# Performance work log

Hardware: AMD Instinct MI355X
Metric: run time of the kernel (lower is better)

The kernel has to match this reference:

```python
import jax, jax.numpy as jnp
import numpy as np

B, S, D, H = 64, 2048, 512, 512


def setup_inputs() -> dict:
    key = jax.random.key(0)
    ks = jax.random.split(key, 8)
    inp = jax.random.normal(ks[0], (B, D), dtype=jnp.float32)
    context = jax.random.normal(ks[1], (B, S, D), dtype=jnp.float32)
    mask = jax.random.randint(ks[2], (B, S), 0, 2).astype(jnp.int32)
    alpha_mask = jax.random.uniform(ks[3], (B, S), dtype=jnp.float32)
    sd = 1.0 / np.sqrt(D)
    W_in = jax.random.uniform(ks[4], (H, D), minval=-sd, maxval=sd, dtype=jnp.float32)
    b_in = jnp.zeros((H,), dtype=jnp.float32)
    W_ctx = jax.random.uniform(ks[5], (H, D), minval=-sd, maxval=sd, dtype=jnp.float32)  # Conv1d k=1 == pointwise linear
    b_ctx = jnp.zeros((H,), dtype=jnp.float32)
    V = jax.random.uniform(ks[6], (H,), minval=-1.0, maxval=1.0, dtype=jnp.float32)
    return {"input": inp, "context": context, "alpha_mask": alpha_mask,
            "W_in": W_in, "b_in": b_in, "W_ctx": W_ctx, "b_ctx": b_ctx, "V": V,
            "mask": mask}


def reference(input, context, alpha_mask, W_in, b_in, W_ctx, b_ctx, V, mask):
    seq_len = context.shape[1]
    # input_linear: [B, H]
    inp = input @ W_in.T + b_in
    # context_linear (Conv1d kernel=1 over permuted context): [B, H, S]
    ctx = jnp.einsum('hd,bsd->bhs', W_ctx, context) + b_ctx[None, :, None]
    # additive attention energies: V . tanh(inp + ctx) -> [B, S]
    att = jnp.einsum('h,bhs->bs', V, jnp.tanh(inp[:, :, None] + ctx))
    # mask branching (faithful to the torch data-dependent branch, jit-safe):
    # if any(mask) and count(mask) == S: att[mask] = -inf; else: att = att * alpha_mask
    mb = mask != 0
    n_true = jnp.sum(mb)
    take_inf_branch = (n_true > 0) & (n_true == seq_len)
    att = jnp.where(take_inf_branch,
                    jnp.where(mb, -jnp.inf, att),
                    att * alpha_mask)
    alpha = jax.nn.softmax(att, axis=-1)  # [B, S]
    # context vector: bmm(ctx [B,H,S], alpha [B,S,1]) -> [B, H]
    hidden_state = jnp.einsum('bhs,bs->bh', ctx, alpha)
    return hidden_state, alpha
```

## Files before the change

### kernel.cpp

```cpp
#include <hip/hip_runtime.h>
#include <math.h>

#define B 64
#define S 2048
#define D 512
#define H 512

#define WSC 128

typedef _Float16 f16x8 __attribute__((ext_vector_type(8)));
typedef __fp16 fp16x2 __attribute__((ext_vector_type(2)));
typedef float f32x4 __attribute__((ext_vector_type(4)));

#define WS_PART_OFF (512 * 1024)
#define WS_CNT_OFF  (512 * 1024 + 2 * 1024 * 1024)

__global__ __launch_bounds__(256) void k_pack_wc(
        const float* __restrict__ Wc, _Float16* __restrict__ wsB,
        int* __restrict__ cnt) {
    if (blockIdx.x == 0 && threadIdx.x == 0) *cnt = 0;
    const int slot = blockIdx.x * 256 + threadIdx.x;
    const int st   = slot >> 11;
    const int rem  = slot & 2047;
    const int hg   = rem >> 6;
    const int lane = rem & 63;
    const int h  = hg * 16 + (lane & 15);
    const int k0 = st * 32 + (lane >> 4) * 8;
    const float* src = Wc + (size_t)h * D + k0;
    float4 f0 = *(const float4*)src;
    float4 f1 = *(const float4*)(src + 4);
    f16x8 v;
    v[0] = (_Float16)f0.x; v[1] = (_Float16)f0.y;
    v[2] = (_Float16)f0.z; v[3] = (_Float16)f0.w;
    v[4] = (_Float16)f1.x; v[5] = (_Float16)f1.y;
    v[6] = (_Float16)f1.z; v[7] = (_Float16)f1.w;
    *(f16x8*)(wsB + (size_t)slot * 8) = v;
}

__global__ __launch_bounds__(256) void k_mask_count(
        const int* __restrict__ mask, int* __restrict__ cnt) {
    const int base = blockIdx.x * 256 + threadIdx.x;
    int local = 0;
    for (int i = base; i < B * S; i += 256 * 64) local += (mask[i] != 0) ? 1 : 0;
    #pragma unroll
    for (int off = 32; off; off >>= 1) local += __shfl_down(local, off, 64);
    if ((threadIdx.x & 63) == 0 && local) atomicAdd(cnt, local);
}

__global__ __launch_bounds__(256) void k_input_linear(
        const float* __restrict__ input,
        const float* __restrict__ W_in,
        const float* __restrict__ b_in,
        float* __restrict__ out_inp) {
    const int b = blockIdx.x;
    const int tid = threadIdx.x;
    __shared__ float xrow[D];
    for (int d = tid; d < D; d += 256) xrow[d] = input[(size_t)b * D + d];
    __syncthreads();
    for (int h = tid; h < H; h += 256) {
        const float* w = W_in + (size_t)h * D;
        float acc = 0.f;
        #pragma unroll 4
        for (int d = 0; d < D; d += 4) {
            float4 wv = *(const float4*)(w + d);
            acc += wv.x * xrow[d] + wv.y * xrow[d + 1] + wv.z * xrow[d + 2] + wv.w * xrow[d + 3];
        }
        out_inp[(size_t)b * H + h] = acc + b_in[h];
    }
}

__global__ __launch_bounds__(512, 4) void k_energy(
        const float* __restrict__ ctx,
        const _Float16* __restrict__ WcP,
        const float* __restrict__ bc,
        const float* __restrict__ inp,
        const float* __restrict__ V,
        float* __restrict__ att) {
    __shared__ alignas(16) _Float16 Alds[64 * 512];
    __shared__ float red[8][64];

    const int tid = threadIdx.x;
    const int b  = blockIdx.x >> 5;
    const int s0 = (blockIdx.x & 31) << 6;

    const int lane = tid & 63;
    const int w    = tid >> 6;
    const int lrow = lane & 15;
    const int kblk = lane >> 4;

    {
        const int row = tid >> 3;
        const int c   = tid & 7;
        const float* src_row = ctx + ((size_t)b * S + s0 + row) * D;
        _Float16* dst_row = &Alds[row * 512];
        const int rsw = row & 7;
        #pragma unroll
        for (int i = 0; i < 8; ++i) {
            const int ls = i * 8 + c;
            float4 f0 = *(const float4*)(src_row + ls * 8);
            float4 f1 = *(const float4*)(src_row + ls * 8 + 4);
            union { fp16x2 h2[4]; f16x8 v; } u;
            u.h2[0] = __builtin_amdgcn_cvt_pkrtz(f0.x, f0.y);
            u.h2[1] = __builtin_amdgcn_cvt_pkrtz(f0.z, f0.w);
            u.h2[2] = __builtin_amdgcn_cvt_pkrtz(f1.x, f1.y);
            u.h2[3] = __builtin_amdgcn_cvt_pkrtz(f1.z, f1.w);
            *(f16x8*)(dst_row + (ls ^ rsw) * 8) = u.v;
        }
    }
    __syncthreads();

    f32x4 acc[4][4] = {};
    const _Float16* Bbase = WcP + ((size_t)(w * 4) * 64 + lane) * 8;
    const int rsw = lrow & 7;

    #pragma unroll 4
    for (int kt = 0; kt < 16; ++kt) {
        f16x8 bfr[4];
        #pragma unroll
        for (int n = 0; n < 4; ++n)
            bfr[n] = *(const f16x8*)(Bbase + ((size_t)kt * 2048 + n * 64) * 8);

        const int ps = (kt * 4 + kblk) ^ rsw;
        f16x8 afr[4];
        #pragma unroll
        for (int m = 0; m < 4; ++m)
            afr[m] = *(const f16x8*)&Alds[(m * 16 + lrow) * 512 + ps * 8];

        #pragma unroll
        for (int m = 0; m < 4; ++m)
            #pragma unroll
            for (int n = 0; n < 4; ++n)
                acc[m][n] = __builtin_amdgcn_mfma_f32_16x16x32_f16(afr[m], bfr[n], acc[m][n], 0, 0, 0);
    }

    float ps_[4][4] = {};
    #pragma unroll
    for (int n = 0; n < 4; ++n) {
        const int h = w * 64 + n * 16 + lrow;
        const float ib = inp[(size_t)b * H + h] + bc[h];
        const float v = V[h];
        #pragma unroll
        for (int m = 0; m < 4; ++m)
            #pragma unroll
            for (int r = 0; r < 4; ++r) {
                const float x = acc[m][n][r] + ib;
                const float t = 1.f - 2.f / (1.f + __expf(2.f * x));
                ps_[m][r] += v * t;
            }
    }
    #pragma unroll
    for (int off = 1; off < 16; off <<= 1)
        #pragma unroll
        for (int m = 0; m < 4; ++m)
            #pragma unroll
            for (int r = 0; r < 4; ++r)
                ps_[m][r] += __shfl_xor(ps_[m][r], off, 64);
    if (lrow == 0) {
        #pragma unroll
        for (int m = 0; m < 4; ++m)
            #pragma unroll
            for (int r = 0; r < 4; ++r)
                red[w][m * 16 + kblk * 4 + r] = ps_[m][r];
    }
    __syncthreads();
    if (tid < 64) {
        float sum = 0.f;
        #pragma unroll
        for (int i = 0; i < 8; ++i) sum += red[i][tid];
        att[(size_t)b * S + s0 + tid] = sum;
    }
}

__global__ __launch_bounds__(256) void k_softmax(
        const int* __restrict__ mask,
        const float* __restrict__ amask,
        const int* __restrict__ cnt,
        float* __restrict__ att) {
    const int b = blockIdx.x;
    const int tid = threadIdx.x;
    __shared__ float sh[S];
    __shared__ float fredm[4];
    __shared__ float freds[4];

    const int n_true = *cnt;
    const bool inf_branch = (n_true > 0) && (n_true == S);

    const float NEG_INF = -__builtin_inff();
    for (int s = tid; s < S; s += 256) {
        const float raw = att[(size_t)b * S + s];
        float v;
        if (inf_branch)
            v = mask[(size_t)b * S + s] ? NEG_INF : raw;
        else
            v = raw * amask[(size_t)b * S + s];
        sh[s] = v;
    }
    __syncthreads();

    float mx = NEG_INF;
    for (int s = tid; s < S; s += 256) mx = fmaxf(mx, sh[s]);
    #pragma unroll
    for (int off = 32; off; off >>= 1) mx = fmaxf(mx, __shfl_down(mx, off, 64));
    if ((tid & 63) == 0) fredm[tid >> 6] = mx;
    __syncthreads();
    mx = fmaxf(fmaxf(fredm[0], fredm[1]), fmaxf(fredm[2], fredm[3]));

    float lsum = 0.f;
    for (int s = tid; s < S; s += 256) {
        const float e = expf(sh[s] - mx);
        sh[s] = e;
        lsum += e;
    }
    #pragma unroll
    for (int off = 32; off; off >>= 1) lsum += __shfl_down(lsum, off, 64);
    if ((tid & 63) == 0) freds[tid >> 6] = lsum;
    __syncthreads();
    const float total = freds[0] + freds[1] + freds[2] + freds[3];
    const float rinv = 1.f / total;

    for (int s = tid; s < S; s += 256)
        att[(size_t)b * S + s] = sh[s] * rinv;
}

__global__ __launch_bounds__(256) void k_wsum(
        const float* __restrict__ ctx,
        const float* __restrict__ alpha,
        float* __restrict__ part) {
    const int chunk = blockIdx.x & 15;
    const int b = blockIdx.x >> 4;
    const int s0 = chunk * WSC;
    const int tid = threadIdx.x;
    __shared__ float al[WSC];
    if (tid < WSC) al[tid] = alpha[(size_t)b * S + s0 + tid];
    __syncthreads();

    const int half = tid >> 7;
    const int dq = (tid & 127) * 4;
    const float* base = ctx + ((size_t)b * S + s0 + half) * D + dq;
    float4 acc = {0.f, 0.f, 0.f, 0.f};
    #pragma unroll 4
    for (int i = 0; i < WSC / 2; ++i) {
        float4 v = *(const float4*)(base + (size_t)i * 2 * D);
        const float a = al[i * 2 + half];
        acc.x += a * v.x; acc.y += a * v.y; acc.z += a * v.z; acc.w += a * v.w;
    }
    __shared__ float cb[2][D];
    *(float4*)&cb[half][dq] = acc;
    __syncthreads();
    if (tid < 128) {
        const int d = tid * 4;
        float4 p0 = *(const float4*)&cb[0][d];
        float4 p1 = *(const float4*)&cb[1][d];
        float4 o = {p0.x + p1.x, p0.y + p1.y, p0.z + p1.z, p0.w + p1.w};
        *(float4*)(part + ((size_t)chunk * B + b) * D + d) = o;
    }
}

__global__ __launch_bounds__(256) void k_out(
        const float* __restrict__ part,
        const float* __restrict__ Wc,
        const float* __restrict__ bc,
        float* __restrict__ hidden) {
    const int b = blockIdx.x;
    const int tid = threadIdx.x;
    __shared__ float cb[D];
    for (int d = tid; d < D; d += 256) {
        float s = 0.f;
        #pragma unroll
        for (int c = 0; c < 16; ++c)
            s += part[((size_t)c * B + b) * D + d];
        cb[d] = s;
    }
    __syncthreads();
    for (int h = tid; h < H; h += 256) {
        const float* w = Wc + (size_t)h * D;
        float acc = 0.f;
        #pragma unroll 4
        for (int d = 0; d < D; d += 4) {
            float4 wv = *(const float4*)(w + d);
            acc += wv.x * cb[d] + wv.y * cb[d + 1] + wv.z * cb[d + 2] + wv.w * cb[d + 3];
        }
        hidden[(size_t)b * H + h] = acc + bc[h];
    }
}

extern "C" void kernel_launch(void* const* d_in, const int* in_sizes, int n_in,
                              void* d_out, int out_size, void* d_ws, size_t ws_size,
                              hipStream_t stream) {
    const float* input = (const float*)d_in[0];
    const float* ctx   = (const float*)d_in[1];
    const float* amask = (const float*)d_in[2];
    const float* W_in  = (const float*)d_in[3];
    const float* b_in  = (const float*)d_in[4];
    const float* W_ctx = (const float*)d_in[5];
    const float* b_ctx = (const float*)d_in[6];
    const float* V     = (const float*)d_in[7];
    const int*   mask  = (const int*)d_in[8];

    float* out = (float*)d_out;
    float* hidden = out;
    float* alpha  = out + B * H;

    _Float16* wsB  = (_Float16*)d_ws;
    float*    part = (float*)((char*)d_ws + WS_PART_OFF);
    int*      cnt  = (int*)((char*)d_ws + WS_CNT_OFF);

    k_pack_wc<<<dim3(128), dim3(256), 0, stream>>>(W_ctx, wsB, cnt);
    k_mask_count<<<dim3(64), dim3(256), 0, stream>>>(mask, cnt);

    k_input_linear<<<dim3(B), dim3(256), 0, stream>>>(input, W_in, b_in, hidden);

    k_energy<<<dim3(B * S / 64), dim3(512), 0, stream>>>(
        ctx, wsB, b_ctx, hidden, V, alpha);

    k_softmax<<<dim3(B), dim3(256), 0, stream>>>(mask, amask, cnt, alpha);

    k_wsum<<<dim3(16 * B), dim3(256), 0, stream>>>(ctx, alpha, part);

    k_out<<<dim3(B), dim3(256), 0, stream>>>(part, W_ctx, b_ctx, hidden);
}
```

Before: 238.5 us.

## Fuse prep kernels, split energy GEMM over H halves with double-buffered LDS pipeline

Merges the W_ctx packing, input linear and mask counting kernels into one launch, with per-block mask counts summed in softmax instead of a global atomic. The energy kernel now uses 256 threads, splits H into two halves per block, and stages both ctx and packed W_ctx K-slices into double-buffered LDS via global_load_lds, overlapping the next slice's loads with MFMA. Partial energies from the two H halves are combined with atomicAdd into a zeroed alpha buffer. This needs an extra memset, reads ctx twice, and gives float-add ordering that is not deterministic.

```diff
diff --git a/kernel.cpp b/kernel.cpp
--- a/kernel.cpp
+++ b/kernel.cpp
@@ -7,136 +7,164 @@
 #define H 512
 
 #define WSC 128
+#define LDA 40
 
 typedef _Float16 f16x8 __attribute__((ext_vector_type(8)));
 typedef __fp16 fp16x2 __attribute__((ext_vector_type(2)));
 typedef float f32x4 __attribute__((ext_vector_type(4)));
 
 #define WS_PART_OFF (512 * 1024)
-#define WS_CNT_OFF  (512 * 1024 + 2 * 1024 * 1024)
-
-__global__ __launch_bounds__(256) void k_pack_wc(
+#define WS_CNT_OFF  (512 * 1024 + 4 * 1024 * 1024)
+
+#define GLOAD16(g, l)                                                          \
+    __builtin_amdgcn_global_load_lds(                                          \
+        (const __attribute__((address_space(1))) uint32_t*)(g),                \
+        (__attribute__((address_space(3))) uint32_t*)(l), 16, 0, 0)
+
+__global__ __launch_bounds__(256) void k_prep(
         const float* __restrict__ Wc, _Float16* __restrict__ wsB,
-        int* __restrict__ cnt) {
-    if (blockIdx.x == 0 && threadIdx.x == 0) *cnt = 0;
-    const int slot = blockIdx.x * 256 + threadIdx.x;
-    const int st   = slot >> 11;
-    const int rem  = slot & 2047;
-    const int hg   = rem >> 6;
-    const int lane = rem & 63;
-    const int h  = hg * 16 + (lane & 15);
-    const int k0 = st * 32 + (lane >> 4) * 8;
-    const float* src = Wc + (size_t)h * D + k0;
-    float4 f0 = *(const float4*)src;
-    float4 f1 = *(const float4*)(src + 4);
-    f16x8 v;
-    v[0] = (_Float16)f0.x; v[1] = (_Float16)f0.y;
-    v[2] = (_Float16)f0.z; v[3] = (_Float16)f0.w;
-    v[4] = (_Float16)f1.x; v[5] = (_Float16)f1.y;
-    v[6] = (_Float16)f1.z; v[7] = (_Float16)f1.w;
-    *(f16x8*)(wsB + (size_t)slot * 8) = v;
-}
-
-__global__ __launch_bounds__(256) void k_mask_count(
-        const int* __restrict__ mask, int* __restrict__ cnt) {
-    const int base = blockIdx.x * 256 + threadIdx.x;
-    int local = 0;
-    for (int i = base; i < B * S; i += 256 * 64) local += (mask[i] != 0) ? 1 : 0;
-    #pragma unroll
-    for (int off = 32; off; off >>= 1) local += __shfl_down(local, off, 64);
-    if ((threadIdx.x & 63) == 0 && local) atomicAdd(cnt, local);
-}
-
-__global__ __launch_bounds__(256) void k_input_linear(
-        const float* __restrict__ input,
-        const float* __restrict__ W_in,
-        const float* __restrict__ b_in,
-        float* __restrict__ out_inp) {
-    const int b = blockIdx.x;
-    const int tid = threadIdx.x;
-    __shared__ float xrow[D];
-    for (int d = tid; d < D; d += 256) xrow[d] = input[(size_t)b * D + d];
-    __syncthreads();
-    for (int h = tid; h < H; h += 256) {
-        const float* w = W_in + (size_t)h * D;
-        float acc = 0.f;
-        #pragma unroll 4
-        for (int d = 0; d < D; d += 4) {
-            float4 wv = *(const float4*)(w + d);
-            acc += wv.x * xrow[d] + wv.y * xrow[d + 1] + wv.z * xrow[d + 2] + wv.w * xrow[d + 3];
+        const float* __restrict__ input, const float* __restrict__ W_in,
+        const float* __restrict__ b_in, float* __restrict__ out_inp,
+        const int* __restrict__ mask, int* __restrict__ cntArr) {
+    const int bid = blockIdx.x;
+    const int tid = threadIdx.x;
+
+    if (bid < 128) {
+        const int slot = bid * 256 + tid;
+        const int st   = slot >> 11;
+        const int rem  = slot & 2047;
+        const int hg   = rem >> 6;
+        const int lane = rem & 63;
+        const int h  = hg * 16 + (lane & 15);
+        const int k0 = st * 32 + (lane >> 4) * 8;
+        const float* src = Wc + (size_t)h * D + k0;
+        float4 f0 = *(const float4*)src;
+        float4 f1 = *(const float4*)(src + 4);
+        f16x8 v;
+        v[0] = (_Float16)f0.x; v[1] = (_Float16)f0.y;
+        v[2] = (_Float16)f0.z; v[3] = (_Float16)f0.w;
+        v[4] = (_Float16)f1.x; v[5] = (_Float16)f1.y;
+        v[6] = (_Float16)f1.z; v[7] = (_Float16)f1.w;
+        *(f16x8*)(wsB + (size_t)slot * 8) = v;
+    } else if (bid < 192) {
+        const int b = bid - 128;
+        __shared__ float xrow[D];
+        for (int d = tid; d < D; d += 256) xrow[d] = input[(size_t)b * D + d];
+        __syncthreads();
+        for (int h = tid; h < H; h += 256) {
+            const float* w = W_in + (size_t)h * D;
+            float acc = 0.f;
+            #pragma unroll 4
+            for (int d = 0; d < D; d += 4) {
+                float4 wv = *(const float4*)(w + d);
+                acc += wv.x * xrow[d] + wv.y * xrow[d + 1] + wv.z * xrow[d + 2] + wv.w * xrow[d + 3];
+            }
+            out_inp[(size_t)b * H + h] = acc + b_in[h];
         }
-        out_inp[(size_t)b * H + h] = acc + b_in[h];
-    }
-}
-
-__global__ __launch_bounds__(512, 4) void k_energy(
+    } else {
+        const int i0 = (bid - 192) * 2048;
+        int local = 0;
+        #pragma unroll
+        for (int it = 0; it < 8; ++it)
+            local += (mask[i0 + it * 256 + tid] != 0) ? 1 : 0;
+        #pragma unroll
+        for (int off = 32; off; off >>= 1) local += __shfl_down(local, off, 64);
+        __shared__ int ired[4];
+        if ((tid & 63) == 0) ired[tid >> 6] = local;
+        __syncthreads();
+        if (tid == 0) cntArr[bid - 192] = ired[0] + ired[1] + ired[2] + ired[3];
+    }
+}
+
+__global__ __launch_bounds__(256) void k_energy(
         const float* __restrict__ ctx,
         const _Float16* __restrict__ WcP,
         const float* __restrict__ bc,
         const float* __restrict__ inp,
         const float* __restrict__ V,
         float* __restrict__ att) {
-    __shared__ alignas(16) _Float16 Alds[64 * 512];
-    __shared__ float red[8][64];
-
-    const int tid = threadIdx.x;
-    const int b  = blockIdx.x >> 5;
-    const int s0 = (blockIdx.x & 31) << 6;
-
+    __shared__ alignas(16) _Float16 Alds[2][64 * LDA];
+    __shared__ alignas(16) _Float16 Blds[2][8192];
+    __shared__ float red[4][64];
+
+    const int tid = threadIdx.x;
+    const int hb    = blockIdx.x & 1;
+    const int stile = blockIdx.x >> 1;
+    const int b  = stile >> 5;
+    const int s0 = (stile & 31) << 6;
+
+    const int arow = tid >> 2;
+    const int akq  = tid & 3;
     const int lane = tid & 63;
     const int w    = tid >> 6;
     const int lrow = lane & 15;
     const int kblk = lane >> 4;
 
+    f32x4 acc[4][4] = {};
+
+    const float* ctx_src = ctx + ((size_t)b * S + s0 + arow) * D + akq * 8;
+    const _Float16* Bg = WcP + ((size_t)(hb * 16 + w * 4) * 64 + lane) * 8;
+
+    #pragma unroll
+    for (int i = 0; i < 4; ++i)
+        GLOAD16(Bg + (size_t)(i * 64) * 8, &Blds[0][(w * 4 + i) * 512]);
     {
-        const int row = tid >> 3;
-        const int c   = tid & 7;
-        const float* src_row = ctx + ((size_t)b * S + s0 + row) * D;
-        _Float16* dst_row = &Alds[row * 512];
-        const int rsw = row & 7;
-        #pragma unroll
-        for (int i = 0; i < 8; ++i) {
-            const int ls = i * 8 + c;
-            float4 f0 = *(const float4*)(src_row + ls * 8);
-            float4 f1 = *(const float4*)(src_row + ls * 8 + 4);
+        float4 f0 = *(const float4*)ctx_src;
+        float4 f1 = *(const float4*)(ctx_src + 4);
+        union { fp16x2 h2[4]; f16x8 v; } u;
+        u.h2[0] = __builtin_amdgcn_cvt_pkrtz(f0.x, f0.y);
+        u.h2[1] = __builtin_amdgcn_cvt_pkrtz(f0.z, f0.w);
+        u.h2[2] = __builtin_amdgcn_cvt_pkrtz(f1.x, f1.y);
+        u.h2[3] = __builtin_amdgcn_cvt_pkrtz(f1.z, f1.w);
+        *(f16x8*)&Alds[0][arow * LDA + akq * 8] = u.v;
+    }
+    __syncthreads();
+
+    #pragma unroll 1
+    for (int kt = 0; kt < 16; ++kt) {
+        const int cur = kt & 1;
+
+        float4 nf0, nf1;
+        if (kt < 15) {
+            #pragma unroll
+            for (int i = 0; i < 4; ++i)
+                GLOAD16(Bg + ((size_t)(kt + 1) * 2048 + i * 64) * 8,
+                        &Blds[cur ^ 1][(w * 4 + i) * 512]);
+            nf0 = *(const float4*)(ctx_src + (kt + 1) * 32);
+            nf1 = *(const float4*)(ctx_src + (kt + 1) * 32 + 4);
+        }
+
+        f16x8 bfr[4];
+        #pragma unroll
+        for (int n = 0; n < 4; ++n)
+            bfr[n] = *(const f16x8*)&Blds[cur][(w * 4 + n) * 512 + lane * 8];
+        f16x8 afr[4];
+        #pragma unroll
+        for (int m = 0; m < 4; ++m)
+            afr[m] = *(const f16x8*)&Alds[cur][(m * 16 + lrow) * LDA + kblk * 8];
+
+        #pragma unroll
+        for (int m = 0; m < 4; ++m)
+            #pragma unroll
+            for (int n = 0; n < 4; ++n)
+                acc[m][n] = __builtin_amdgcn_mfma_f32_16x16x32_f16(
+                    afr[m], bfr[n], acc[m][n], 0, 0, 0);
+
+        if (kt < 15) {
             union { fp16x2 h2[4]; f16x8 v; } u;
-            u.h2[0] = __builtin_amdgcn_cvt_pkrtz(f0.x, f0.y);
-            u.h2[1] = __builtin_amdgcn_cvt_pkrtz(f0.z, f0.w);
-            u.h2[2] = __builtin_amdgcn_cvt_pkrtz(f1.x, f1.y);
-            u.h2[3] = __builtin_amdgcn_cvt_pkrtz(f1.z, f1.w);
-            *(f16x8*)(dst_row + (ls ^ rsw) * 8) = u.v;
+            u.h2[0] = __builtin_amdgcn_cvt_pkrtz(nf0.x, nf0.y);
+            u.h2[1] = __builtin_amdgcn_cvt_pkrtz(nf0.z, nf0.w);
+            u.h2[2] = __builtin_amdgcn_cvt_pkrtz(nf1.x, nf1.y);
+            u.h2[3] = __builtin_amdgcn_cvt_pkrtz(nf1.z, nf1.w);
+            *(f16x8*)&Alds[cur ^ 1][arow * LDA + akq * 8] = u.v;
         }
-    }
-    __syncthreads();
-
-    f32x4 acc[4][4] = {};
-    const _Float16* Bbase = WcP + ((size_t)(w * 4) * 64 + lane) * 8;
-    const int rsw = lrow & 7;
-
-    #pragma unroll 4
-    for (int kt = 0; kt < 16; ++kt) {
-        f16x8 bfr[4];
-        #pragma unroll
-        for (int n = 0; n < 4; ++n)
-            bfr[n] = *(const f16x8*)(Bbase + ((size_t)kt * 2048 + n * 64) * 8);
-
-        const int ps = (kt * 4 + kblk) ^ rsw;
-        f16x8 afr[4];
-        #pragma unroll
-        for (int m = 0; m < 4; ++m)
-            afr[m] = *(const f16x8*)&Alds[(m * 16 + lrow) * 512 + ps * 8];
-
-        #pragma unroll
-        for (int m = 0; m < 4; ++m)
-            #pragma unroll
-            for (int n = 0; n < 4; ++n)
-                acc[m][n] = __builtin_amdgcn_mfma_f32_16x16x32_f16(afr[m], bfr[n], acc[m][n], 0, 0, 0);
+        __syncthreads();
     }
 
     float ps_[4][4] = {};
     #pragma unroll
     for (int n = 0; n < 4; ++n) {
-        const int h = w * 64 + n * 16 + lrow;
+        const int h = hb * 256 + (w * 4 + n) * 16 + lrow;
         const float ib = inp[(size_t)b * H + h] + bc[h];
         const float v = V[h];
         #pragma unroll
@@ -164,17 +192,15 @@
     }
     __syncthreads();
     if (tid < 64) {
-        float sum = 0.f;
-        #pragma unroll
-        for (int i = 0; i < 8; ++i) sum += red[i][tid];
-        att[(size_t)b * S + s0 + tid] = sum;
+        const float sum = red[0][tid] + red[1][tid] + red[2][tid] + red[3][tid];
+        atomicAdd(att + (size_t)b * S + s0 + tid, sum);
     }
 }
 
 __global__ __launch_bounds__(256) void k_softmax(
         const int* __restrict__ mask,
         const float* __restrict__ amask,
-        const int* __restrict__ cnt,
+        const int* __restrict__ cntArr,
         float* __restrict__ att) {
     const int b = blockIdx.x;
     const int tid = threadIdx.x;
@@ -182,7 +208,9 @@
     __shared__ float fredm[4];
     __shared__ float freds[4];
 
-    const int n_true = *cnt;
+    int n_true = 0;
+    #pragma unroll
+    for (int i = 0; i < 64; ++i) n_true += cntArr[i];
     const bool inf_branch = (n_true > 0) && (n_true == S);
 
     const float NEG_INF = -__builtin_inff();
@@ -301,19 +329,18 @@
     float* hidden = out;
     float* alpha  = out + B * H;
 
-    _Float16* wsB  = (_Float16*)d_ws;
-    float*    part = (float*)((char*)d_ws + WS_PART_OFF);
-    int*      cnt  = (int*)((char*)d_ws + WS_CNT_OFF);
-
-    k_pack_wc<<<dim3(128), dim3(256), 0, stream>>>(W_ctx, wsB, cnt);
-    k_mask_count<<<dim3(64), dim3(256), 0, stream>>>(mask, cnt);
-
-    k_input_linear<<<dim3(B), dim3(256), 0, stream>>>(input, W_in, b_in, hidden);
-
-    k_energy<<<dim3(B * S / 64), dim3(512), 0, stream>>>(
+    _Float16* wsB    = (_Float16*)d_ws;
+    float*    part   = (float*)((char*)d_ws + WS_PART_OFF);
+    int*      cntArr = (int*)((char*)d_ws + WS_CNT_OFF);
+
+    k_prep<<<dim3(256), dim3(256), 0, stream>>>(
+        W_ctx, wsB, input, W_in, b_in, hidden, mask, cntArr);
+
+    (void)hipMemsetAsync(alpha, 0, (size_t)B * S * sizeof(float), stream);
+    k_energy<<<dim3(B * S / 64 * 2), dim3(256), 0, stream>>>(
         ctx, wsB, b_ctx, hidden, V, alpha);
 
-    k_softmax<<<dim3(B), dim3(256), 0, stream>>>(mask, amask, cnt, alpha);
+    k_softmax<<<dim3(B), dim3(256), 0, stream>>>(mask, amask, cntArr, alpha);
 
     k_wsum<<<dim3(16 * B), dim3(256), 0, stream>>>(ctx, alpha, part);
 
```

Result: slower. 251.9 us (+5.6%).
